# Kernel tuning notes

Hardware: AMD Instinct MI355X
Metric: run time of the kernel (lower is better)

The kernel has to match this reference:

```python
import jax, jax.numpy as jnp
import numpy as np

N, E, B = 100000, 1200000, 512
IN_DIM, HID, K, NCLS = 64, 64, 3, 10


def setup_inputs() -> dict:
    key = jax.random.key(0)
    ks = jax.random.split(key, 10)
    features = jax.random.normal(ks[0], (N, IN_DIM), jnp.float32)
    edge_src = jax.random.randint(ks[1], (E,), 0, N)
    edge_dst = jax.random.randint(ks[2], (E,), 0, N)
    graph_ids = jnp.sort(jax.random.randint(ks[3], (N,), 0, B))
    s1 = float(1.0 / np.sqrt(IN_DIM))
    W1 = jax.random.uniform(ks[4], (IN_DIM, HID), jnp.float32, -s1, s1)
    b1 = jnp.zeros((HID,), jnp.float32)
    s2 = float(1.0 / np.sqrt(HID))
    W2 = jax.random.uniform(ks[5], (HID, HID), jnp.float32, -s2, s2)
    b2 = jnp.zeros((HID,), jnp.float32)
    s3 = float(1.0 / np.sqrt(HID * 3))
    cw = jax.random.uniform(ks[6], (HID, HID, 3), jnp.float32, -s3, s3)
    cb = jax.random.uniform(ks[7], (HID,), jnp.float32, -s3, s3)
    Wc = jax.random.uniform(ks[8], (HID, NCLS), jnp.float32, -s2, s2)
    bc = jax.random.uniform(ks[9], (NCLS,), jnp.float32, -s2, s2)
    return dict(features=features, edge_src=edge_src, edge_dst=edge_dst,
                graph_ids=graph_ids, num_graphs=B,
                W1=W1, b1=b1, W2=W2, b2=b2, cw=cw, cb=cb, Wc=Wc, bc=bc)


def graph_conv(h, src, dst, W, b, n_nodes):
    # DGL GraphConv, norm='both', allow_zero_in_degree (degrees clamped to 1)
    ones = jnp.ones((src.shape[0],), h.dtype)
    out_deg = jnp.zeros((n_nodes,), h.dtype).at[src].add(ones)
    in_deg = jnp.zeros((n_nodes,), h.dtype).at[dst].add(ones)
    norm_s = jax.lax.rsqrt(jnp.clip(out_deg, 1.0, None))
    norm_d = jax.lax.rsqrt(jnp.clip(in_deg, 1.0, None))
    m = (h * norm_s[:, None]) @ W  # weight first; math identical to agg-first
    agg = jnp.zeros((n_nodes, W.shape[1]), h.dtype).at[dst].add(m[src])
    return agg * norm_d[:, None] + b


def sort_pool(h, gid, num_graphs, k):
    # DGL SortPooling: sort each node's features ascending along feature dim,
    # then take top-k nodes per graph by last feature value (descending),
    # zero-padding graphs with < k nodes. Output [num_graphs, k*D].
    hs = jnp.sort(h, axis=-1)
    key = hs[:, -1]
    order = jnp.lexsort((-key, gid))  # gid asc, key desc
    gid_s = gid[order]
    hs_s = hs[order]
    n = gid.shape[0]
    start = jnp.full((num_graphs,), n).at[gid_s].min(jnp.arange(n))
    rank = jnp.arange(n) - start[gid_s]  # within-graph rank by key desc
    mask = rank < k
    slot = gid_s * k + jnp.clip(rank, 0, k - 1)
    out = jnp.zeros((num_graphs * k, hs.shape[-1]), h.dtype).at[slot].add(
        jnp.where(mask[:, None], hs_s, jnp.zeros((), h.dtype)))
    return out.reshape(num_graphs, k * hs.shape[-1])


def reference(features, edge_src, edge_dst, graph_ids, num_graphs,
              W1, b1, W2, b2, cw, cb, Wc, bc):
    n = features.shape[0]
    h = jax.nn.relu(graph_conv(features, edge_src, edge_dst, W1, b1, n))
    h = jax.nn.relu(graph_conv(h, edge_src, edge_dst, W2, b2, n))
    p = sort_pool(h, graph_ids, num_graphs, K)          # [B, K*HID]
    x = p.reshape(num_graphs, HID, K)                    # faithful torch reshape
    # Conv1d(kernel=3, stride=1) on length-3 input -> length-1 output
    y = jax.nn.relu(jnp.einsum('bct,oct->bo', x, cw) + cb)
    return y @ Wc + bc
```

## Files before the change

### kernel.cpp

```cpp
#include <hip/hip_runtime.h>
#include <hip/hip_bf16.h>


#define PART_H 50176
#define QPART_H (PART_H / 4)
#define PART_F 25088
#define QUART_F (PART_F / 4)
#define MCH  128
#define MCHS 32

__global__ void __launch_bounds__(256) k_histgemm(
    const int* __restrict__ esrc, const int* __restrict__ edst,
    unsigned char* __restrict__ hd, unsigned char* __restrict__ hs,
    const float* __restrict__ in, const float* __restrict__ W,
    float* __restrict__ mout, int N, int E, int PH, int histBlocks) {
  __shared__ float smem[12800];
  const int t = threadIdx.x;
  if (blockIdx.x < histBlocks) {
    unsigned int* lc = (unsigned int*)smem;
    const int b = blockIdx.x;
    const int dblk = PH * MCH;
    const int a = (b < dblk) ? 0 : 1;
    const int r = a ? (b - dblk) : b;
    const int mch = a ? MCHS : MCH;
    const int p = r % PH;
    const int m = r / PH;
    const int* __restrict__ arr = a ? esrc : edst;
    unsigned char* __restrict__ outp = a ? hs : hd;
    const int base = p * PART_H;
    const int lim = min(PART_H, N - base);
    {
      uint4 z = make_uint4(0u, 0u, 0u, 0u);
      uint4* lc16 = (uint4*)lc;
      for (int i = t; i < QPART_H / 4; i += 256) lc16[i] = z;
    }
    __syncthreads();
    const long long cb = (long long)m * E / mch;
    const long long ce = (long long)(m + 1) * E / mch;
    const long long a0 = min((cb + 3) & ~3LL, ce);
    const long long nv = (ce - a0) >> 2;
    for (long long e = cb + t; e < a0; e += 256) {
      int d = arr[e] - base;
      if ((unsigned)d < (unsigned)lim) atomicAdd(&lc[d >> 2], 1u << ((d & 3) * 8));
    }
    const int4* __restrict__ a4p = (const int4*)(arr + a0);
    for (long long i = t; i < nv; i += 256) {
      int4 v4 = a4p[i];
      int d;
      d = v4.x - base; if ((unsigned)d < (unsigned)lim) atomicAdd(&lc[d >> 2], 1u << ((d & 3) * 8));
      d = v4.y - base; if ((unsigned)d < (unsigned)lim) atomicAdd(&lc[d >> 2], 1u << ((d & 3) * 8));
      d = v4.z - base; if ((unsigned)d < (unsigned)lim) atomicAdd(&lc[d >> 2], 1u << ((d & 3) * 8));
      d = v4.w - base; if ((unsigned)d < (unsigned)lim) atomicAdd(&lc[d >> 2], 1u << ((d & 3) * 8));
    }
    for (long long e = a0 + (nv << 2) + t; e < ce; e += 256) {
      int d = arr[e] - base;
      if ((unsigned)d < (unsigned)lim) atomicAdd(&lc[d >> 2], 1u << ((d & 3) * 8));
    }
    __syncthreads();
    unsigned char* slice = outp + ((size_t)p * mch + m) * PART_H;
    uint4* slice16 = (uint4*)slice;
    const uint4* lc16 = (const uint4*)lc;
    for (int i = t; i < QPART_H / 4; i += 256) slice16[i] = lc16[i];
  } else {
    float* Wl = smem;
    float* Ac = smem + 4096;
    const int ch = (t & 7) * 8;
    const int nb = (t >> 3) * 4;
    for (int i = t; i < 1024; i += 256)
      ((float4*)Wl)[i] = ((const float4*)W)[i];
    const int gb = blockIdx.x - histBlocks;
    const int ng = gridDim.x - histBlocks;
    const int NT = (N + 127) >> 7;
    for (int tile = gb; tile < NT; tile += ng) {
      const int vbase = tile << 7;
      __syncthreads();
      for (int i = t; i < 2048; i += 256) {
        const int r = i >> 4;
        const int c = (i & 15) * 4;
        const int v = vbase + r;
        float4 val = make_float4(0.f, 0.f, 0.f, 0.f);
        if (v < N) val = *(const float4*)(in + (size_t)v * 64 + c);
        Ac[(c + 0) * 136 + r] = val.x;
        Ac[(c + 1) * 136 + r] = val.y;
        Ac[(c + 2) * 136 + r] = val.z;
        Ac[(c + 3) * 136 + r] = val.w;
      }
      __syncthreads();
      float acc[4][8];
#pragma unroll
      for (int j = 0; j < 4; ++j)
#pragma unroll
        for (int c = 0; c < 8; ++c) acc[j][c] = 0.f;
      for (int k = 0; k < 64; k += 4) {
#pragma unroll
        for (int kk = 0; kk < 4; ++kk) {
          const float4 aa = *(const float4*)&Ac[(k + kk) * 136 + nb];
          const float4 w0 = *(const float4*)&Wl[(k + kk) * 64 + ch];
          const float4 w1 = *(const float4*)&Wl[(k + kk) * 64 + ch + 4];
          const float an[4] = {aa.x, aa.y, aa.z, aa.w};
          const float wn[8] = {w0.x, w0.y, w0.z, w0.w, w1.x, w1.y, w1.z, w1.w};
#pragma unroll
          for (int j = 0; j < 4; ++j)
#pragma unroll
            for (int c = 0; c < 8; ++c)
              acc[j][c] = fmaf(an[j], wn[c], acc[j][c]);
        }
      }
#pragma unroll
      for (int j = 0; j < 4; ++j) {
        const int v = vbase + nb + j;
        if (v < N) {
          float4 o0, o1;
          o0.x = acc[j][0]; o0.y = acc[j][1]; o0.z = acc[j][2]; o0.w = acc[j][3];
          o1.x = acc[j][4]; o1.y = acc[j][5]; o1.z = acc[j][6]; o1.w = acc[j][7];
          *(float4*)(mout + (size_t)v * 64 + ch)     = o0;
          *(float4*)(mout + (size_t)v * 64 + ch + 4) = o1;
        }
      }
    }
  }
}

__global__ void __launch_bounds__(256) k_offscan(
    unsigned char* __restrict__ hd, const unsigned char* __restrict__ hs,
    int* __restrict__ deg_d, float* __restrict__ norm_s, float* __restrict__ norm_d,
    int* __restrict__ gstart, int* __restrict__ rowptr, int* __restrict__ bsum,
    int B, int N) {
  __shared__ unsigned long long part[32][8];
  __shared__ unsigned long long spart[32][8];
  __shared__ int sums[256];
  const int t = threadIdx.x;
  const int s = t >> 3;
  const int c = t & 7;
  const int nb0 = blockIdx.x * 256;
  const int v0 = nb0 + s * 8;
  const int vt = nb0 + t;
  if (vt < B) gstart[vt] = 0x7f7f7f7f;
  const size_t rb  = (size_t)(v0 / PART_H) * MCH  * PART_H + (size_t)(v0 % PART_H);
  const size_t rbs = (size_t)(v0 / PART_H) * MCHS * PART_H + (size_t)(v0 % PART_H);
  unsigned long long* __restrict__ hd8 = (unsigned long long*)(hd + rb);
  const unsigned long long* __restrict__ hs8 = (const unsigned long long*)(hs + rbs);
  const size_t st8 = PART_H / 8;
  const int m0 = c * 16;
  const int m0s = c * 4;
  const bool act = (v0 < N);
  unsigned long long vals[16];
  unsigned long long tsum = 0ull, hsum = 0ull;
  if (act) {
#pragma unroll
    for (int k = 0; k < 16; ++k) {
      vals[k] = hd8[(size_t)(m0 + k) * st8];
      tsum += vals[k];
    }
#pragma unroll
    for (int k = 0; k < 4; ++k) hsum += hs8[(size_t)(m0s + k) * st8];
  }
  part[s][c] = tsum;
  spart[s][c] = hsum;
  __syncthreads();
  if (act) {
    unsigned long long run = 0ull;
#pragma unroll
    for (int cc = 0; cc < 8; ++cc)
      if (cc < c) run += part[s][cc];
#pragma unroll
    for (int k = 0; k < 16; ++k) {
      const unsigned long long w = vals[k];
      hd8[(size_t)(m0 + k) * st8] = run;
      run += w;
    }
  }
  unsigned long long dt = 0ull, ht = 0ull;
#pragma unroll
  for (int cc = 0; cc < 8; ++cc) {
    dt += part[t >> 3][cc];
    ht += spart[t >> 3][cc];
  }
  int dg = 0;
  if (vt < N) {
    dg = (int)((dt >> (8 * (t & 7))) & 0xffull);
    const int so = (int)((ht >> (8 * (t & 7))) & 0xffull);
    deg_d[vt] = dg;
    norm_d[vt] = rsqrtf((float)max(dg, 1));
    norm_s[vt] = rsqrtf((float)max(so, 1));
  }
  sums[t] = dg;
  __syncthreads();
  for (int off = 1; off < 256; off <<= 1) {
    int x = (t >= off) ? sums[t - off] : 0;
    __syncthreads();
    sums[t] += x;
    __syncthreads();
  }
  if (vt < N) rowptr[vt] = sums[t] - dg;
  if (t == 255) bsum[blockIdx.x] = sums[255];
}

__global__ void k_scan2(int* __restrict__ bsum, int nb) {
  __shared__ int sh[512];
  const int t = threadIdx.x;
  const int v = (t < nb) ? bsum[t] : 0;
  sh[t] = v;
  __syncthreads();
  for (int off = 1; off < 512; off <<= 1) {
    int x = (t >= off) ? sh[t - off] : 0;
    __syncthreads();
    sh[t] += x;
    __syncthreads();
  }
  if (t < nb) bsum[t] = sh[t] - v;
}

__global__ void k_fill2(const int* __restrict__ esrc, const int* __restrict__ edst,
                        const unsigned char* __restrict__ hd, const int* __restrict__ rowptr,
                        const int* __restrict__ bsum, int* __restrict__ csr,
                        int N, int E, int PF) {
  __shared__ unsigned int cur4[QUART_F];
  const int b = blockIdx.x;
  const int p = b % PF;
  const int m = b / PF;
  const int base = p * PART_F;
  const int lim = min(PART_F, N - base);
  const unsigned char* slice = hd + ((size_t)(p >> 1) * MCH + m) * PART_H
                                  + (size_t)(p & 1) * PART_F;
  const unsigned int* slice4 = (const unsigned int*)slice;
  for (int i = threadIdx.x; i < QUART_F; i += blockDim.x) cur4[i] = slice4[i];
  __syncthreads();
  const int* __restrict__ rp = rowptr + base;
  const long long cb = (long long)m * E / MCH;
  const long long ce = (long long)(m + 1) * E / MCH;
  const long long a0 = min((cb + 3) & ~3LL, ce);
  const long long nv = (ce - a0) >> 2;
  for (long long e = cb + threadIdx.x; e < a0; e += blockDim.x) {
    int d = edst[e] - base;
    if ((unsigned)d < (unsigned)lim) {
      unsigned int old = atomicAdd(&cur4[d >> 2], 1u << ((d & 3) * 8));
      csr[rp[d] + bsum[(base + d) >> 8] + ((old >> ((d & 3) * 8)) & 0xff)] = esrc[e];
    }
  }
  const int4* __restrict__ d4p = (const int4*)(edst + a0);
  const int4* __restrict__ s4p = (const int4*)(esrc + a0);
  for (long long i = threadIdx.x; i < nv; i += blockDim.x) {
    int4 d4 = d4p[i];
    int4 s4 = s4p[i];
    int d;
    d = d4.x - base;
    if ((unsigned)d < (unsigned)lim) {
      unsigned int old = atomicAdd(&cur4[d >> 2], 1u << ((d & 3) * 8));
      csr[rp[d] + bsum[(base + d) >> 8] + ((old >> ((d & 3) * 8)) & 0xff)] = s4.x;
    }
    d = d4.y - base;
    if ((unsigned)d < (unsigned)lim) {
      unsigned int old = atomicAdd(&cur4[d >> 2], 1u << ((d & 3) * 8));
      csr[rp[d] + bsum[(base + d) >> 8] + ((old >> ((d & 3) * 8)) & 0xff)] = s4.y;
    }
    d = d4.z - base;
    if ((unsigned)d < (unsigned)lim) {
      unsigned int old = atomicAdd(&cur4[d >> 2], 1u << ((d & 3) * 8));
      csr[rp[d] + bsum[(base + d) >> 8] + ((old >> ((d & 3) * 8)) & 0xff)] = s4.z;
    }
    d = d4.w - base;
    if ((unsigned)d < (unsigned)lim) {
      unsigned int old = atomicAdd(&cur4[d >> 2], 1u << ((d & 3) * 8));
      csr[rp[d] + bsum[(base + d) >> 8] + ((old >> ((d & 3) * 8)) & 0xff)] = s4.w;
    }
  }
  for (long long e = a0 + (nv << 2) + threadIdx.x; e < ce; e += blockDim.x) {
    int d = edst[e] - base;
    if ((unsigned)d < (unsigned)lim) {
      unsigned int old = atomicAdd(&cur4[d >> 2], 1u << ((d & 3) * 8));
      csr[rp[d] + bsum[(base + d) >> 8] + ((old >> ((d & 3) * 8)) & 0xff)] = esrc[e];
    }
  }
}

__global__ void __launch_bounds__(256) k_gemm64(
    const float* __restrict__ in, const float* __restrict__ norm,
    const float* __restrict__ W, float* __restrict__ out, int N) {
  __shared__ float Wl[4096];
  __shared__ float Ac[64 * 136];
  const int t = threadIdx.x;
  const int ch = (t & 7) * 8;
  const int nb = (t >> 3) * 4;
  for (int i = t; i < 1024; i += 256)
    ((float4*)Wl)[i] = ((const float4*)W)[i];
  const int NT = (N + 127) >> 7;
  for (int tile = blockIdx.x; tile < NT; tile += gridDim.x) {
    const int vbase = tile << 7;
    __syncthreads();
    for (int i = t; i < 2048; i += 256) {
      const int r = i >> 4;
      const int c = (i & 15) * 4;
      const int v = vbase + r;
      float4 val = make_float4(0.f, 0.f, 0.f, 0.f);
      if (v < N) val = *(const float4*)(in + (size_t)v * 64 + c);
      Ac[(c + 0) * 136 + r] = val.x;
      Ac[(c + 1) * 136 + r] = val.y;
      Ac[(c + 2) * 136 + r] = val.z;
      Ac[(c + 3) * 136 + r] = val.w;
    }
    __syncthreads();
    float acc[4][8];
#pragma unroll
    for (int j = 0; j < 4; ++j)
#pragma unroll
      for (int c = 0; c < 8; ++c) acc[j][c] = 0.f;
    for (int k = 0; k < 64; k += 4) {
#pragma unroll
      for (int kk = 0; kk < 4; ++kk) {
        const float4 aa = *(const float4*)&Ac[(k + kk) * 136 + nb];
        const float4 w0 = *(const float4*)&Wl[(k + kk) * 64 + ch];
        const float4 w1 = *(const float4*)&Wl[(k + kk) * 64 + ch + 4];
        const float an[4] = {aa.x, aa.y, aa.z, aa.w};
        const float wn[8] = {w0.x, w0.y, w0.z, w0.w, w1.x, w1.y, w1.z, w1.w};
#pragma unroll
        for (int j = 0; j < 4; ++j)
#pragma unroll
          for (int c = 0; c < 8; ++c)
            acc[j][c] = fmaf(an[j], wn[c], acc[j][c]);
      }
    }
#pragma unroll
    for (int j = 0; j < 4; ++j) {
      const int v = vbase + nb + j;
      if (v < N) {
        const float nm = norm[v];
        float4 o0, o1;
        o0.x = acc[j][0] * nm; o0.y = acc[j][1] * nm;
        o0.z = acc[j][2] * nm; o0.w = acc[j][3] * nm;
        o1.x = acc[j][4] * nm; o1.y = acc[j][5] * nm;
        o1.z = acc[j][6] * nm; o1.w = acc[j][7] * nm;
        *(float4*)(out + (size_t)v * 64 + ch)     = o0;
        *(float4*)(out + (size_t)v * 64 + ch + 4) = o1;
      }
    }
  }
}

__global__ void k_gather(const float* __restrict__ m, const int* __restrict__ rowptr,
                         const int* __restrict__ bsum,
                         const int* __restrict__ deg, const float* __restrict__ norm_d,
                         const float* __restrict__ bias, const int* __restrict__ csr,
                         const float* __restrict__ nsrc,
                         const int* __restrict__ gid, int* __restrict__ gstart,
                         float* __restrict__ h, float* __restrict__ key, int N) {
  const int wpb = blockDim.x >> 6;
  const int nwaves = gridDim.x * wpb;
  const int lane = threadIdx.x & 63;
  const int chb = (lane & 7) * 8;
  const int grp = lane >> 3;
  const float4 b0 = *(const float4*)(bias + chb);
  const float4 b1 = *(const float4*)(bias + chb + 4);
  for (int w = blockIdx.x * wpb + (threadIdx.x >> 6); w < N; w += nwaves) {
    if (gid != nullptr && lane == 0) {
      int g = gid[w];
      if (w == 0 || gid[w - 1] != g) gstart[g] = w;
    }
    const int start = rowptr[w] + bsum[w >> 8];
    const int cnt = deg[w];
    float4 a00 = make_float4(0.f, 0.f, 0.f, 0.f);
    float4 a01 = make_float4(0.f, 0.f, 0.f, 0.f);
    float4 a10 = make_float4(0.f, 0.f, 0.f, 0.f);
    float4 a11 = make_float4(0.f, 0.f, 0.f, 0.f);
    int i = grp;
    if (nsrc != nullptr) {
      for (; i + 8 < cnt; i += 16) {
        int s0 = csr[start + i];
        int s1 = csr[start + i + 8];
        float n0 = nsrc[s0], n1 = nsrc[s1];
        const float* r0 = m + (size_t)s0 * 64 + chb;
        const float* r1 = m + (size_t)s1 * 64 + chb;
        const float4 v00 = *(const float4*)r0;
        const float4 v01 = *(const float4*)(r0 + 4);
        const float4 v10 = *(const float4*)r1;
        const float4 v11 = *(const float4*)(r1 + 4);
        a00.x = fmaf(v00.x, n0, a00.x); a00.y = fmaf(v00.y, n0, a00.y);
        a00.z = fmaf(v00.z, n0, a00.z); a00.w = fmaf(v00.w, n0, a00.w);
        a01.x = fmaf(v01.x, n0, a01.x); a01.y = fmaf(v01.y, n0, a01.y);
        a01.z = fmaf(v01.z, n0, a01.z); a01.w = fmaf(v01.w, n0, a01.w);
        a10.x = fmaf(v10.x, n1, a10.x); a10.y = fmaf(v10.y, n1, a10.y);
        a10.z = fmaf(v10.z, n1, a10.z); a10.w = fmaf(v10.w, n1, a10.w);
        a11.x = fmaf(v11.x, n1, a11.x); a11.y = fmaf(v11.y, n1, a11.y);
        a11.z = fmaf(v11.z, n1, a11.z); a11.w = fmaf(v11.w, n1, a11.w);
      }
      if (i < cnt) {
        int s0 = csr[start + i];
        float n0 = nsrc[s0];
        const float* r0 = m + (size_t)s0 * 64 + chb;
        const float4 v00 = *(const float4*)r0;
        const float4 v01 = *(const float4*)(r0 + 4);
        a00.x = fmaf(v00.x, n0, a00.x); a00.y = fmaf(v00.y, n0, a00.y);
        a00.z = fmaf(v00.z, n0, a00.z); a00.w = fmaf(v00.w, n0, a00.w);
        a01.x = fmaf(v01.x, n0, a01.x); a01.y = fmaf(v01.y, n0, a01.y);
        a01.z = fmaf(v01.z, n0, a01.z); a01.w = fmaf(v01.w, n0, a01.w);
      }
    } else {
      for (; i + 8 < cnt; i += 16) {
        int s0 = csr[start + i];
        int s1 = csr[start + i + 8];
        const float* r0 = m + (size_t)s0 * 64 + chb;
        const float* r1 = m + (size_t)s1 * 64 + chb;
        const float4 v00 = *(const float4*)r0;
        const float4 v01 = *(const float4*)(r0 + 4);
        const float4 v10 = *(const float4*)r1;
        const float4 v11 = *(const float4*)(r1 + 4);
        a00.x += v00.x; a00.y += v00.y; a00.z += v00.z; a00.w += v00.w;
        a01.x += v01.x; a01.y += v01.y; a01.z += v01.z; a01.w += v01.w;
        a10.x += v10.x; a10.y += v10.y; a10.z += v10.z; a10.w += v10.w;
        a11.x += v11.x; a11.y += v11.y; a11.z += v11.z; a11.w += v11.w;
      }
      if (i < cnt) {
        int s0 = csr[start + i];
        const float* r0 = m + (size_t)s0 * 64 + chb;
        const float4 v00 = *(const float4*)r0;
        const float4 v01 = *(const float4*)(r0 + 4);
        a00.x += v00.x; a00.y += v00.y; a00.z += v00.z; a00.w += v00.w;
        a01.x += v01.x; a01.y += v01.y; a01.z += v01.z; a01.w += v01.w;
      }
    }
    a00.x += a10.x; a00.y += a10.y; a00.z += a10.z; a00.w += a10.w;
    a01.x += a11.x; a01.y += a11.y; a01.z += a11.z; a01.w += a11.w;
#pragma unroll
    for (int off = 8; off <= 32; off <<= 1) {
      a00.x += __shfl_xor(a00.x, off, 64);
      a00.y += __shfl_xor(a00.y, off, 64);
      a00.z += __shfl_xor(a00.z, off, 64);
      a00.w += __shfl_xor(a00.w, off, 64);
      a01.x += __shfl_xor(a01.x, off, 64);
      a01.y += __shfl_xor(a01.y, off, 64);
      a01.z += __shfl_xor(a01.z, off, 64);
      a01.w += __shfl_xor(a01.w, off, 64);
    }
    const float nd = norm_d[w];
    float4 o0, o1;
    o0.x = fmaxf(fmaf(a00.x, nd, b0.x), 0.f);
    o0.y = fmaxf(fmaf(a00.y, nd, b0.y), 0.f);
    o0.z = fmaxf(fmaf(a00.z, nd, b0.z), 0.f);
    o0.w = fmaxf(fmaf(a00.w, nd, b0.w), 0.f);
    o1.x = fmaxf(fmaf(a01.x, nd, b1.x), 0.f);
    o1.y = fmaxf(fmaf(a01.y, nd, b1.y), 0.f);
    o1.z = fmaxf(fmaf(a01.z, nd, b1.z), 0.f);
    o1.w = fmaxf(fmaf(a01.w, nd, b1.w), 0.f);
    if (h != nullptr && grp == 0) {
      *(float4*)(h + (size_t)w * 64 + chb)     = o0;
      *(float4*)(h + (size_t)w * 64 + chb + 4) = o1;
    }
    if (key != nullptr) {
      float mx = fmaxf(fmaxf(fmaxf(o0.x, o0.y), fmaxf(o0.z, o0.w)),
                       fmaxf(fmaxf(o1.x, o1.y), fmaxf(o1.z, o1.w)));
#pragma unroll
      for (int off = 1; off < 8; off <<= 1) mx = fmaxf(mx, __shfl_xor(mx, off, 64));
      if (lane == 0) key[w] = mx;
    }
  }
}

__global__ void __launch_bounds__(256) k_tail(
    const float* __restrict__ key, const int* __restrict__ gstart,
    const float* __restrict__ m, const int* __restrict__ rowptr,
    const int* __restrict__ bsum, const int* __restrict__ deg,
    const float* __restrict__ norm_d, const float* __restrict__ bias,
    const int* __restrict__ csr,
    const float* __restrict__ cw, const float* __restrict__ cb,
    const float* __restrict__ Wc, const float* __restrict__ bc,
    float* __restrict__ out, int B, int N) {
  __shared__ int sel[3];
  __shared__ float prow[192];
  const int b = blockIdx.x;
  const int wid = threadIdx.x >> 6;
  const int lane = threadIdx.x & 63;

  if (wid == 0) {
    const int gs = gstart[b];
    int g2 = b + 1;
    while (g2 < B && gstart[g2] >= N) ++g2;
    const int ns = (g2 < B) ? gstart[g2] : N;
    const int s = gs;
    const int c = (gs < N) ? (ns - gs) : 0;
    float v0 = -1.f, v1 = -1.f, v2 = -1.f;
    int i0 = 0x7fffffff, i1 = 0x7fffffff, i2 = 0x7fffffff;
    for (int i = s + lane; i < s + c; i += 64) {
      float kv = key[i];
      if (kv > v0 || (kv == v0 && i < i0)) {
        v2 = v1; i2 = i1; v1 = v0; i1 = i0; v0 = kv; i0 = i;
      } else if (kv > v1 || (kv == v1 && i < i1)) {
        v2 = v1; i2 = i1; v1 = kv; i1 = i;
      } else if (kv > v2 || (kv == v2 && i < i2)) {
        v2 = kv; i2 = i;
      }
    }
    int ptr = 0;
    for (int r = 0; r < 3; ++r) {
      float mv = (ptr == 0) ? v0 : (ptr == 1) ? v1 : (ptr == 2) ? v2 : -1.f;
      int   mi = (ptr == 0) ? i0 : (ptr == 1) ? i1 : (ptr == 2) ? i2 : 0x7fffffff;
      float bv = mv; int bi = mi;
#pragma unroll
      for (int off = 32; off; off >>= 1) {
        float ov = __shfl_xor(bv, off, 64);
        int   oi = __shfl_xor(bi, off, 64);
        if (ov > bv || (ov == bv && oi < bi)) { bv = ov; bi = oi; }
      }
      if (bi == mi && ptr < 3) ptr++;
      if (lane == 0) sel[r] = (bi == 0x7fffffff) ? -1 : bi;
    }
  }
  __syncthreads();
  if (wid < 3) {
    const int node = sel[wid];
    if (node >= 0) {
      const int chb = (lane & 7) * 8;
      const int grp = lane >> 3;
      const int start = rowptr[node] + bsum[node >> 8];
      const int cnt = deg[node];
      float4 a00 = make_float4(0.f, 0.f, 0.f, 0.f);
      float4 a01 = make_float4(0.f, 0.f, 0.f, 0.f);
      float4 a10 = make_float4(0.f, 0.f, 0.f, 0.f);
      float4 a11 = make_float4(0.f, 0.f, 0.f, 0.f);
      int i = grp;
      for (; i + 8 < cnt; i += 16) {
        int s0 = csr[start + i];
        int s1 = csr[start + i + 8];
        const float* r0 = m + (size_t)s0 * 64 + chb;
        const float* r1 = m + (size_t)s1 * 64 + chb;
        const float4 v00 = *(const float4*)r0;
        const float4 v01 = *(const float4*)(r0 + 4);
        const float4 v10 = *(const float4*)r1;
        const float4 v11 = *(const float4*)(r1 + 4);
        a00.x += v00.x; a00.y += v00.y; a00.z += v00.z; a00.w += v00.w;
        a01.x += v01.x; a01.y += v01.y; a01.z += v01.z; a01.w += v01.w;
        a10.x += v10.x; a10.y += v10.y; a10.z += v10.z; a10.w += v10.w;
        a11.x += v11.x; a11.y += v11.y; a11.z += v11.z; a11.w += v11.w;
      }
      if (i < cnt) {
        int s0 = csr[start + i];
        const float* r0 = m + (size_t)s0 * 64 + chb;
        const float4 v00 = *(const float4*)r0;
        const float4 v01 = *(const float4*)(r0 + 4);
        a00.x += v00.x; a00.y += v00.y; a00.z += v00.z; a00.w += v00.w;
        a01.x += v01.x; a01.y += v01.y; a01.z += v01.z; a01.w += v01.w;
      }
      a00.x += a10.x; a00.y += a10.y; a00.z += a10.z; a00.w += a10.w;
      a01.x += a11.x; a01.y += a11.y; a01.z += a11.z; a01.w += a11.w;
#pragma unroll
      for (int off = 8; off <= 32; off <<= 1) {
        a00.x += __shfl_xor(a00.x, off, 64);
        a00.y += __shfl_xor(a00.y, off, 64);
        a00.z += __shfl_xor(a00.z, off, 64);
        a00.w += __shfl_xor(a00.w, off, 64);
        a01.x += __shfl_xor(a01.x, off, 64);
        a01.y += __shfl_xor(a01.y, off, 64);
        a01.z += __shfl_xor(a01.z, off, 64);
        a01.w += __shfl_xor(a01.w, off, 64);
      }
      const float nd = norm_d[node];
      const float4 b0 = *(const float4*)(bias + chb);
      const float4 b1 = *(const float4*)(bias + chb + 4);
      float4 o0, o1;
      o0.x = fmaxf(fmaf(a00.x, nd, b0.x), 0.f);
      o0.y = fmaxf(fmaf(a00.y, nd, b0.y), 0.f);
      o0.z = fmaxf(fmaf(a00.z, nd, b0.z), 0.f);
      o0.w = fmaxf(fmaf(a00.w, nd, b0.w), 0.f);
      o1.x = fmaxf(fmaf(a01.x, nd, b1.x), 0.f);
      o1.y = fmaxf(fmaf(a01.y, nd, b1.y), 0.f);
      o1.z = fmaxf(fmaf(a01.z, nd, b1.z), 0.f);
      o1.w = fmaxf(fmaf(a01.w, nd, b1.w), 0.f);
      if (grp == 0) {
        *(float4*)&prow[wid * 64 + chb]     = o0;
        *(float4*)&prow[wid * 64 + chb + 4] = o1;
      }
    } else {
      prow[wid * 64 + lane] = 0.f;
    }
  }
  __syncthreads();
  if (wid < 3) {
    float v = prow[wid * 64 + lane];
    if (sel[wid] >= 0) {
      for (int k2 = 2; k2 <= 64; k2 <<= 1) {
        for (int j = k2 >> 1; j > 0; j >>= 1) {
          float o = __shfl_xor(v, j, 64);
          bool up = ((lane & k2) == 0);
          bool lower = ((lane & j) == 0);
          v = (lower == up) ? fminf(v, o) : fmaxf(v, o);
        }
      }
    }
    prow[wid * 64 + lane] = v;
  }
  __syncthreads();
  if (wid == 0) {
    float y = cb[lane];
    for (int j = 0; j < 192; ++j) y = fmaf(prow[j], cw[lane * 192 + j], y);
    float ry = fmaxf(y, 0.f);
    for (int c = 0; c < 10; ++c) {
      float s = ry * Wc[lane * 10 + c];
#pragma unroll
      for (int off = 32; off; off >>= 1) s += __shfl_xor(s, off, 64);
      if (lane == 0) out[b * 10 + c] = s + bc[c];
    }
  }
}

extern "C" void kernel_launch(void* const* d_in, const int* in_sizes, int n_in,
                              void* d_out, int out_size, void* d_ws, size_t ws_size,
                              hipStream_t stream) {
  const float* features = (const float*)d_in[0];
  const int*   esrc     = (const int*)d_in[1];
  const int*   edst     = (const int*)d_in[2];
  const int*   gid      = (const int*)d_in[3];
  const float* W1 = (const float*)d_in[5];
  const float* b1 = (const float*)d_in[6];
  const float* W2 = (const float*)d_in[7];
  const float* b2 = (const float*)d_in[8];
  const float* cw = (const float*)d_in[9];
  const float* cb = (const float*)d_in[10];
  const float* Wc = (const float*)d_in[11];
  const float* bc = (const float*)d_in[12];
  float* out = (float*)d_out;

  const int N = in_sizes[0] / 64;
  const int E = in_sizes[1];
  const int B = out_size / 10;
  const size_t N64 = (size_t)N * 64;
  const int nscan = (N + 255) / 256;
  const int PH = (N + PART_H - 1) / PART_H;
  const int PF = (N + PART_F - 1) / PART_F;
  const size_t HSZD = (size_t)PH * MCH  * PART_H;
  const size_t HSZS = (size_t)PH * MCHS * PART_H;
  const int NT = (N + 127) / 128;
  const int histBlocks = PH * (MCH + MCHS);

  float* bufA   = (float*)d_ws;
  float* bufB   = bufA + N64;
  int*   deg_d  = (int*)(bufB + N64);
  float* norm_s = (float*)(deg_d + N);
  float* norm_d = norm_s + N;
  float* key    = norm_d + N;
  int*   rowptr = (int*)(key + N);
  int*   csr    = rowptr + N;
  int*   bsum   = csr + E;
  int*   gstart = bsum + 512;
  unsigned char* hd = (unsigned char*)(((size_t)(gstart + B) + 15) & ~(size_t)15);
  unsigned char* hs = hd + HSZD;

  const int TB = 256;

  k_histgemm<<<histBlocks + NT, TB, 0, stream>>>(esrc, edst, hd, hs,
                                                 features, W1, bufA,
                                                 N, E, PH, histBlocks);
  k_offscan<<<nscan, 256, 0, stream>>>(hd, hs, deg_d, norm_s, norm_d,
                                       gstart, rowptr, bsum, B, N);
  k_scan2<<<1, 512, 0, stream>>>(bsum, nscan);
  k_fill2<<<PF * MCH, TB, 0, stream>>>(esrc, edst, hd, rowptr, bsum, csr, N, E, PF);

  const int GB = 2048;

  k_gather<<<GB, TB, 0, stream>>>(bufA, rowptr, bsum, deg_d, norm_d, b1,
                                  csr, norm_s, nullptr, nullptr,
                                  bufB, nullptr, N);

  k_gemm64<<<NT, TB, 0, stream>>>(bufB, norm_s, W2, bufA, N);
  k_gather<<<GB, TB, 0, stream>>>(bufA, rowptr, bsum, deg_d, norm_d, b2,
                                  csr, nullptr, gid, gstart,
                                  nullptr, key, N);

  k_tail<<<B, TB, 0, stream>>>(key, gstart, bufA, rowptr, bsum, deg_d,
                               norm_d, b2, csr, cw, cb, Wc, bc, out, B, N);
}
```

Measured before the change: 286.8 us.

## Pack degree histograms into 4-bit counters covering all nodes per block

Each histogram block now keeps 4-bit counters for every node in shared memory, so it no longer splits nodes into 8-bit partitions. Each edge chunk is scanned once instead of once per partition, and histBlocks shrinks from PH*(MCH+MCHS) to MCH+MCHS. The offset-scan kernel unpacks the nibbles to bytes and writes an 8-bit offset histogram into a separate buffer for the fill kernel. The risk is a 4-bit overflow if any node gets more than 15 edges within one chunk, and fewer blocks each do more atomics on a larger shared array.

```diff
diff --git a/kernel.cpp b/kernel.cpp
--- a/kernel.cpp
+++ b/kernel.cpp
@@ -2,37 +2,41 @@
 #include <hip/hip_bf16.h>
 
 
-#define PART_H 50176
-#define QPART_H (PART_H / 4)
 #define PART_F 25088
 #define QUART_F (PART_F / 4)
 #define MCH  128
 #define MCHS 32
 
+__device__ __forceinline__ unsigned long long nib2b(unsigned int x) {
+  unsigned long long lo = x & 0x0F0F0F0Fu;
+  unsigned long long hi = (x >> 4) & 0x0F0F0F0Fu;
+  lo = (lo | (lo << 16)) & 0x0000FFFF0000FFFFull;
+  lo = (lo | (lo << 8))  & 0x00FF00FF00FF00FFull;
+  hi = (hi | (hi << 16)) & 0x0000FFFF0000FFFFull;
+  hi = (hi | (hi << 8))  & 0x00FF00FF00FF00FFull;
+  return lo | (hi << 8);
+}
+
 __global__ void __launch_bounds__(256) k_histgemm(
     const int* __restrict__ esrc, const int* __restrict__ edst,
-    unsigned char* __restrict__ hd, unsigned char* __restrict__ hs,
+    unsigned char* __restrict__ hd4, unsigned char* __restrict__ hs4,
     const float* __restrict__ in, const float* __restrict__ W,
-    float* __restrict__ mout, int N, int E, int PH, int histBlocks) {
+    float* __restrict__ mout, int N, int E, int NP, int histBlocks) {
   __shared__ float smem[12800];
   const int t = threadIdx.x;
   if (blockIdx.x < histBlocks) {
     unsigned int* lc = (unsigned int*)smem;
     const int b = blockIdx.x;
-    const int dblk = PH * MCH;
-    const int a = (b < dblk) ? 0 : 1;
-    const int r = a ? (b - dblk) : b;
+    const int a = (b < MCH) ? 0 : 1;
+    const int m = a ? (b - MCH) : b;
     const int mch = a ? MCHS : MCH;
-    const int p = r % PH;
-    const int m = r / PH;
     const int* __restrict__ arr = a ? esrc : edst;
-    unsigned char* __restrict__ outp = a ? hs : hd;
-    const int base = p * PART_H;
-    const int lim = min(PART_H, N - base);
+    unsigned char* __restrict__ outp = a ? hs4 : hd4;
+    const int nq = NP >> 5;
     {
       uint4 z = make_uint4(0u, 0u, 0u, 0u);
       uint4* lc16 = (uint4*)lc;
-      for (int i = t; i < QPART_H / 4; i += 256) lc16[i] = z;
+      for (int i = t; i < nq; i += 256) lc16[i] = z;
     }
     __syncthreads();
     const long long cb = (long long)m * E / mch;
@@ -40,27 +44,25 @@
     const long long a0 = min((cb + 3) & ~3LL, ce);
     const long long nv = (ce - a0) >> 2;
     for (long long e = cb + t; e < a0; e += 256) {
-      int d = arr[e] - base;
-      if ((unsigned)d < (unsigned)lim) atomicAdd(&lc[d >> 2], 1u << ((d & 3) * 8));
+      int d = arr[e];
+      atomicAdd(&lc[d >> 3], 1u << ((d & 7) * 4));
     }
     const int4* __restrict__ a4p = (const int4*)(arr + a0);
     for (long long i = t; i < nv; i += 256) {
       int4 v4 = a4p[i];
-      int d;
-      d = v4.x - base; if ((unsigned)d < (unsigned)lim) atomicAdd(&lc[d >> 2], 1u << ((d & 3) * 8));
-      d = v4.y - base; if ((unsigned)d < (unsigned)lim) atomicAdd(&lc[d >> 2], 1u << ((d & 3) * 8));
-      d = v4.z - base; if ((unsigned)d < (unsigned)lim) atomicAdd(&lc[d >> 2], 1u << ((d & 3) * 8));
-      d = v4.w - base; if ((unsigned)d < (unsigned)lim) atomicAdd(&lc[d >> 2], 1u << ((d & 3) * 8));
+      atomicAdd(&lc[v4.x >> 3], 1u << ((v4.x & 7) * 4));
+      atomicAdd(&lc[v4.y >> 3], 1u << ((v4.y & 7) * 4));
+      atomicAdd(&lc[v4.z >> 3], 1u << ((v4.z & 7) * 4));
+      atomicAdd(&lc[v4.w >> 3], 1u << ((v4.w & 7) * 4));
     }
     for (long long e = a0 + (nv << 2) + t; e < ce; e += 256) {
-      int d = arr[e] - base;
-      if ((unsigned)d < (unsigned)lim) atomicAdd(&lc[d >> 2], 1u << ((d & 3) * 8));
-    }
-    __syncthreads();
-    unsigned char* slice = outp + ((size_t)p * mch + m) * PART_H;
-    uint4* slice16 = (uint4*)slice;
+      int d = arr[e];
+      atomicAdd(&lc[d >> 3], 1u << ((d & 7) * 4));
+    }
+    __syncthreads();
+    uint4* slice16 = (uint4*)(outp + (size_t)m * (NP >> 1));
     const uint4* lc16 = (const uint4*)lc;
-    for (int i = t; i < QPART_H / 4; i += 256) slice16[i] = lc16[i];
+    for (int i = t; i < nq; i += 256) slice16[i] = lc16[i];
   } else {
     float* Wl = smem;
     float* Ac = smem + 4096;
@@ -122,10 +124,11 @@
 }
 
 __global__ void __launch_bounds__(256) k_offscan(
-    unsigned char* __restrict__ hd, const unsigned char* __restrict__ hs,
+    const unsigned char* __restrict__ hd4, const unsigned char* __restrict__ hs4,
+    unsigned char* __restrict__ hd8,
     int* __restrict__ deg_d, float* __restrict__ norm_s, float* __restrict__ norm_d,
     int* __restrict__ gstart, int* __restrict__ rowptr, int* __restrict__ bsum,
-    int B, int N) {
+    int B, int N, int NP) {
   __shared__ unsigned long long part[32][8];
   __shared__ unsigned long long spart[32][8];
   __shared__ int sums[256];
@@ -136,38 +139,36 @@
   const int v0 = nb0 + s * 8;
   const int vt = nb0 + t;
   if (vt < B) gstart[vt] = 0x7f7f7f7f;
-  const size_t rb  = (size_t)(v0 / PART_H) * MCH  * PART_H + (size_t)(v0 % PART_H);
-  const size_t rbs = (size_t)(v0 / PART_H) * MCHS * PART_H + (size_t)(v0 % PART_H);
-  unsigned long long* __restrict__ hd8 = (unsigned long long*)(hd + rb);
-  const unsigned long long* __restrict__ hs8 = (const unsigned long long*)(hs + rbs);
-  const size_t st8 = PART_H / 8;
+  const size_t half = (size_t)(NP >> 1);
+  const unsigned char* __restrict__ hdp = hd4 + (v0 >> 1);
+  const unsigned char* __restrict__ hsp = hs4 + (v0 >> 1);
   const int m0 = c * 16;
   const int m0s = c * 4;
-  const bool act = (v0 < N);
   unsigned long long vals[16];
   unsigned long long tsum = 0ull, hsum = 0ull;
-  if (act) {
-#pragma unroll
-    for (int k = 0; k < 16; ++k) {
-      vals[k] = hd8[(size_t)(m0 + k) * st8];
-      tsum += vals[k];
-    }
-#pragma unroll
-    for (int k = 0; k < 4; ++k) hsum += hs8[(size_t)(m0s + k) * st8];
+#pragma unroll
+  for (int k = 0; k < 16; ++k) {
+    unsigned int x = *(const unsigned int*)(hdp + (size_t)(m0 + k) * half);
+    vals[k] = nib2b(x);
+    tsum += vals[k];
+  }
+#pragma unroll
+  for (int k = 0; k < 4; ++k) {
+    unsigned int x = *(const unsigned int*)(hsp + (size_t)(m0s + k) * half);
+    hsum += nib2b(x);
   }
   part[s][c] = tsum;
   spart[s][c] = hsum;
   __syncthreads();
-  if (act) {
+  {
     unsigned long long run = 0ull;
 #pragma unroll
     for (int cc = 0; cc < 8; ++cc)
       if (cc < c) run += part[s][cc];
 #pragma unroll
     for (int k = 0; k < 16; ++k) {
-      const unsigned long long w = vals[k];
-      hd8[(size_t)(m0 + k) * st8] = run;
-      run += w;
+      *(unsigned long long*)(hd8 + (size_t)(m0 + k) * NP + v0) = run;
+      run += vals[k];
     }
   }
   unsigned long long dt = 0ull, ht = 0ull;
@@ -212,17 +213,16 @@
 }
 
 __global__ void k_fill2(const int* __restrict__ esrc, const int* __restrict__ edst,
-                        const unsigned char* __restrict__ hd, const int* __restrict__ rowptr,
+                        const unsigned char* __restrict__ hd8, const int* __restrict__ rowptr,
                         const int* __restrict__ bsum, int* __restrict__ csr,
-                        int N, int E, int PF) {
+                        int N, int E, int PF, int NP) {
   __shared__ unsigned int cur4[QUART_F];
   const int b = blockIdx.x;
   const int p = b % PF;
   const int m = b / PF;
   const int base = p * PART_F;
   const int lim = min(PART_F, N - base);
-  const unsigned char* slice = hd + ((size_t)(p >> 1) * MCH + m) * PART_H
-                                  + (size_t)(p & 1) * PART_F;
+  const unsigned char* slice = hd8 + (size_t)m * NP + (size_t)p * PART_F;
   const unsigned int* slice4 = (const unsigned int*)slice;
   for (int i = threadIdx.x; i < QUART_F; i += blockDim.x) cur4[i] = slice4[i];
   __syncthreads();
@@ -623,12 +623,10 @@
   const int B = out_size / 10;
   const size_t N64 = (size_t)N * 64;
   const int nscan = (N + 255) / 256;
-  const int PH = (N + PART_H - 1) / PART_H;
   const int PF = (N + PART_F - 1) / PART_F;
-  const size_t HSZD = (size_t)PH * MCH  * PART_H;
-  const size_t HSZS = (size_t)PH * MCHS * PART_H;
+  const int NP = PF * PART_F;
   const int NT = (N + 127) / 128;
-  const int histBlocks = PH * (MCH + MCHS);
+  const int histBlocks = MCH + MCHS;
 
   float* bufA   = (float*)d_ws;
   float* bufB   = bufA + N64;
@@ -640,18 +638,20 @@
   int*   csr    = rowptr + N;
   int*   bsum   = csr + E;
   int*   gstart = bsum + 512;
-  unsigned char* hd = (unsigned char*)(((size_t)(gstart + B) + 15) & ~(size_t)15);
-  unsigned char* hs = hd + HSZD;
+  unsigned char* hd4 = (unsigned char*)(((size_t)(gstart + B) + 15) & ~(size_t)15);
+  unsigned char* hs4 = hd4 + (size_t)MCH  * (NP >> 1);
+  unsigned char* hd8 = hs4 + (size_t)MCHS * (NP >> 1);
 
   const int TB = 256;
 
-  k_histgemm<<<histBlocks + NT, TB, 0, stream>>>(esrc, edst, hd, hs,
+  k_histgemm<<<histBlocks + NT, TB, 0, stream>>>(esrc, edst, hd4, hs4,
                                                  features, W1, bufA,
-                                                 N, E, PH, histBlocks);
-  k_offscan<<<nscan, 256, 0, stream>>>(hd, hs, deg_d, norm_s, norm_d,
-                                       gstart, rowptr, bsum, B, N);
+                                                 N, E, NP, histBlocks);
+  k_offscan<<<nscan, 256, 0, stream>>>(hd4, hs4, hd8, deg_d, norm_s, norm_d,
+                                       gstart, rowptr, bsum, B, N, NP);
   k_scan2<<<1, 512, 0, stream>>>(bsum, nscan);
-  k_fill2<<<PF * MCH, TB, 0, stream>>>(esrc, edst, hd, rowptr, bsum, csr, N, E, PF);
+  k_fill2<<<PF * MCH, TB, 0, stream>>>(esrc, edst, hd8, rowptr, bsum, csr,
+                                       N, E, PF, NP);
 
   const int GB = 2048;
 
```

After: 296.8 us. +3.5%, slower.
